# Performance work log

Measured on AMD Instinct MI355X. Metric: run time of the kernel, lower is better.

Reference implementation:

```python
import jax, jax.numpy as jnp
import numpy as np

P, N, NF = 4, 871, 512            # num_meta_paths, node_size (hardcoded 871 in source), node_feature_size
XDIM = 116 * 116                   # x_proj input dim, hardcoded Linear(116*116, nf)
BETA, LAMBDA_WL, GAMMA = 0.1, 0.1, 0.1


def _xavier(k, shape):
    fan_in, fan_out = shape[0], shape[-1]
    bound = np.sqrt(6.0 / (fan_in + fan_out))
    return jax.random.uniform(k, shape, jnp.float32, -bound, bound)


def setup_inputs() -> dict:
    key = jax.random.key(0)
    ks = jax.random.split(key, 12)
    return {
        "z_stack": jax.random.normal(ks[0], (P, N, NF), jnp.float32),
        "x_orig": jax.random.normal(ks[1], (1, 116, 116), jnp.float32),
        "W": _xavier(ks[2], (N, 1)),
        "b": jax.random.uniform(ks[3], (N, 1), jnp.float32),
        "q": _xavier(ks[4], (N, NF)),
        "xp_w": _xavier(ks[5], (XDIM, NF)),
        "xp_b": jnp.zeros((NF,), jnp.float32),
        "w1": _xavier(ks[6], (2 * NF, 512)), "b1": jnp.zeros((512,), jnp.float32),
        "w2": _xavier(ks[7], (512, 256)), "b2": jnp.zeros((256,), jnp.float32),
        "w3": _xavier(ks[8], (256, 1)), "b3": jnp.zeros((1,), jnp.float32),
        "perm": jax.random.permutation(ks[9], N).astype(jnp.int32),
    }


def _mi_mlp(t, w1, b1, w2, b2, w3, b3):
    h = jax.nn.relu(t @ w1 + b1)
    h = jax.nn.relu(h @ w2 + b2)
    return h @ w3 + b3  # [N, 1]


def reference(z_stack, x_orig, W, b, q, xp_w, xp_b, w1, b1, w2, b2, w3, b3, perm):
    # --- vectorized form of the per-node loop:
    # score_p = mean_i( tanh(W_i * z[p,i,:] + b_i) . q_i )
    zt = jnp.tanh(W[None] * z_stack + b[None])            # [P,N,NF]
    scores = jnp.mean(jnp.sum(zt * q[None], axis=-1), axis=-1)  # [P]
    proportions = scores / jnp.sum(scores)
    attn = jax.nn.softmax(proportions)                    # [P] (no isomorphic pairs -> no overwrite)
    # layer_out_p = attn_p * z_p + z_p ; emb = sum_p layer_out_p
    emb = jnp.einsum('p,pnf->nf', 1.0 + attn, z_stack)    # [N,NF]
    # --- estimate_MI(x_orig, emb, mi_estimator_xz)
    x = jnp.broadcast_to(x_orig.reshape(1, -1), (N, XDIM))
    xh = x @ xp_w + xp_b                                  # [N,NF]
    t0 = jnp.concatenate([xh, emb], axis=1)               # [N,2NF]
    t1 = jnp.concatenate([xh, emb[perm]], axis=1)
    mi_lb = jnp.mean(_mi_mlp(t0, w1, b1, w2, b2, w3, b3)) - jnp.log(
        jnp.mean(jnp.exp(_mi_mlp(t1, w1, b1, w2, b2, w3, b3))) + 1e-8)
    I_XZ = jnp.clip(mi_lb, 0.0)
    # y_labels=None -> I_ZY = 0 ; empty isomorphic_pairs -> wl_loss = 0
    total_loss = I_XZ - BETA * 0.0 + LAMBDA_WL * 0.0 + GAMMA * jnp.sum(attn)
    return emb, total_loss
```

## Files before the change

kernel.cpp:

```cpp
#include <hip/hip_runtime.h>
#include <hip/hip_bf16.h>
#include <math.h>

#define NMETA  4
#define NNODE  871
#define NFEAT  512
#define XDIM   (116*116)
#define ZPLANE (NNODE*NFEAT)
#define MT     55

#define NXB    254
#define XROWS  53

#define WS_CNT    12
#define WS_SPART  16
#define WS_C1P    256
#define WS_XHP    2560
#define WS_V      132608
#define WS_W1P    133504
#define WS_W2P    264576
#define WS_FXHP   297344
#define MAGICF    0x13579BDFu

typedef short v8s __attribute__((ext_vector_type(8)));
typedef float v4f __attribute__((ext_vector_type(4)));

static __device__ __forceinline__ short f2bf(float f) {
  __hip_bfloat16 h = __float2bfloat16(f);
  return *reinterpret_cast<short*>(&h);
}

static __device__ __forceinline__ unsigned ldflag(const float* ws, int off) {
  return __hip_atomic_load((const unsigned*)&ws[off], __ATOMIC_RELAXED,
                           __HIP_MEMORY_SCOPE_AGENT);
}
static __device__ __forceinline__ void stflag(float* ws, int off) {
  __builtin_amdgcn_fence(__ATOMIC_RELEASE, "agent");
  __hip_atomic_store((unsigned*)&ws[off], MAGICF, __ATOMIC_RELAXED,
                     __HIP_MEMORY_SCOPE_AGENT);
}

__global__ __launch_bounds__(1024) void k_front(const float* __restrict__ x,
                                                const float* __restrict__ xpw,
                                                const float* __restrict__ w1,
                                                const float* __restrict__ w2,
                                                const float* __restrict__ z,
                                                const float* __restrict__ W,
                                                const float* __restrict__ b,
                                                const float* __restrict__ q,
                                                const float* __restrict__ xpb,
                                                const float* __restrict__ b1,
                                                float* __restrict__ ws,
                                                short* __restrict__ w1p,
                                                short* __restrict__ w2p) {
  const int blk = blockIdx.x;
  const int tid = threadIdx.x;

  if (blk < NXB) {
    const int d0 = blk * XROWS;
    const int rows = min(XROWS, XDIM - d0);
    __shared__ float xs[XROWS];
    __shared__ float4 redx[7][128];
    if (tid < rows) xs[tid] = x[d0 + tid];
    __syncthreads();
    const int f4 = tid & 127;
    const int g = tid >> 7;
    float4 acc = {0.f, 0.f, 0.f, 0.f};
    const float4* xp4 = (const float4*)xpw;
    for (int r = g; r < rows; r += 8) {
      const float xv = xs[r];
      const float4 wv = xp4[(size_t)(d0 + r) * 128 + f4];
      acc.x += xv * wv.x; acc.y += xv * wv.y; acc.z += xv * wv.z; acc.w += xv * wv.w;
    }
    if (g) redx[g - 1][f4] = acc;
    __syncthreads();
    if (!g) {
#pragma unroll
      for (int k = 0; k < 7; ++k) {
        float4 t = redx[k][f4];
        acc.x += t.x; acc.y += t.y; acc.z += t.z; acc.w += t.w;
      }
      ((float4*)(ws + WS_XHP + (size_t)blk * 512))[f4] = acc;
    }
    __syncthreads();
    if (tid == 0) stflag(ws, WS_FXHP + blk);
  } else if (blk < NXB + MT) {
    const int sb = blk - NXB;
    const int row = tid >> 6;
    const int oc = tid & 63;
    const int gr = sb * 16 + row;
    const bool valid = gr < NNODE;
    const float4* z4 = (const float4*)z;
    const float4* q4 = (const float4*)q;
    float4 za0, za1, zb0, zb1, zc0, zc1, zd0, zd1, qa, qb;
    float wi = 0.f, bi = 0.f;
    za0 = za1 = zb0 = zb1 = zc0 = zc1 = zd0 = zd1 = (float4){0,0,0,0};
    qa = qb = (float4){0,0,0,0};
    const int zi = gr * 128 + oc * 2;
    if (valid) {
      za0 = z4[zi];                 za1 = z4[zi + 1];
      zb0 = z4[NNODE*128 + zi];     zb1 = z4[NNODE*128 + zi + 1];
      zc0 = z4[2*NNODE*128 + zi];   zc1 = z4[2*NNODE*128 + zi + 1];
      zd0 = z4[3*NNODE*128 + zi];   zd1 = z4[3*NNODE*128 + zi + 1];
      qa  = q4[zi];                 qb  = q4[zi + 1];
      wi = W[gr]; bi = b[gr];
    }
    auto dot8 = [&](const float4& u0, const float4& u1) -> float {
      return tanhf(wi*u0.x + bi)*qa.x + tanhf(wi*u0.y + bi)*qa.y
           + tanhf(wi*u0.z + bi)*qa.z + tanhf(wi*u0.w + bi)*qa.w
           + tanhf(wi*u1.x + bi)*qb.x + tanhf(wi*u1.y + bi)*qb.y
           + tanhf(wi*u1.z + bi)*qb.z + tanhf(wi*u1.w + bi)*qb.w;
    };
    float sp0 = valid ? dot8(za0, za1) : 0.f;
    float sp1 = valid ? dot8(zb0, zb1) : 0.f;
    float sp2 = valid ? dot8(zc0, zc1) : 0.f;
    float sp3 = valid ? dot8(zd0, zd1) : 0.f;
#pragma unroll
    for (int m = 1; m < 64; m <<= 1) {
      sp0 += __shfl_xor(sp0, m); sp1 += __shfl_xor(sp1, m);
      sp2 += __shfl_xor(sp2, m); sp3 += __shfl_xor(sp3, m);
    }
    __shared__ float sred[16][4];
    if (oc == 0) {
      sred[row][0] = sp0; sred[row][1] = sp1;
      sred[row][2] = sp2; sred[row][3] = sp3;
    }
    __syncthreads();
    if (tid < 4) {
      float s = 0.f;
#pragma unroll
      for (int r = 0; r < 16; ++r) s += sred[r][tid];
      ws[WS_SPART + tid * 55 + sb] = s;
    }
  } else if (blk < NXB + MT + 20) {
    const int pb = blk - (NXB + MT);
    if (pb < 16) {
      const int s0 = pb * 16384;
#pragma unroll
      for (int it = 0; it < 16; ++it) {
        const int s = s0 + it * 1024 + tid;
        const int k = s >> 9, n = s & 511;
        const int t = (k >> 5) * 16384 + (n >> 4) * 512 + ((k >> 3) & 3) * 128
                    + (n & 15) * 8 + (k & 7);
        w1p[t] = f2bf(w1[(size_t)(512 + k) * 512 + n]);
      }
    } else {
      const int o0 = (pb - 16) * 16384;
#pragma unroll
      for (int it = 0; it < 16; ++it) {
        const int o = o0 + it * 1024 + tid;
        const int k = o >> 8, n = o & 255;
        const int t = (k >> 5) * 8192 + (n >> 4) * 512 + ((k >> 3) & 3) * 128
                    + (n & 15) * 8 + (k & 7);
        w2p[t] = f2bf(w2[(size_t)k * 256 + n]);
      }
    }
  } else {
    const int bk = blk - (NXB + MT + 20);
    __shared__ float xh[128];
    __shared__ float redr[1024];
    __shared__ float4 redg[7][128];
    if (tid == 1023) *(unsigned*)&ws[WS_CNT] = 0u;
    for (;;) {
      int ok = 1;
      if (tid < NXB) ok = (ldflag(ws, WS_FXHP + tid) == MAGICF);
      if (__syncthreads_and(ok)) break;
      __builtin_amdgcn_s_sleep(2);
    }
    __builtin_amdgcn_fence(__ATOMIC_ACQUIRE, "agent");
    const int f = tid & 127;
    const int part = tid >> 7;
    {
      float s = 0.f;
      for (int p = part; p < NXB; p += 8)
        s += ws[WS_XHP + (size_t)p * 512 + bk * 128 + f];
      redr[tid] = s;
    }
    __syncthreads();
    if (tid < 128) {
      float t = xpb[bk * 128 + tid];
#pragma unroll
      for (int g = 0; g < 8; ++g) t += redr[g * 128 + tid];
      xh[tid] = t;
    }
    __syncthreads();
    const int j4 = tid & 127;
    const int fg = tid >> 7;
    float4 acc = {0.f, 0.f, 0.f, 0.f};
    const float4* w14 = (const float4*)w1;
#pragma unroll
    for (int ff = 0; ff < 16; ++ff) {
      const int fr = bk * 128 + fg * 16 + ff;
      const float xv = xh[fg * 16 + ff];
      const float4 wv = w14[(size_t)fr * 128 + j4];
      acc.x += xv * wv.x; acc.y += xv * wv.y; acc.z += xv * wv.z; acc.w += xv * wv.w;
    }
    if (fg) redg[fg - 1][j4] = acc;
    __syncthreads();
    if (!fg) {
#pragma unroll
      for (int g = 0; g < 7; ++g) {
        float4 t = redg[g][j4];
        acc.x += t.x; acc.y += t.y; acc.z += t.z; acc.w += t.w;
      }
      if (bk == 0) {
        acc.x += b1[j4 * 4 + 0]; acc.y += b1[j4 * 4 + 1];
        acc.z += b1[j4 * 4 + 2]; acc.w += b1[j4 * 4 + 3];
      }
      ((float4*)(ws + WS_C1P + (size_t)bk * 512))[j4] = acc;
    }
  }
}

__global__ __launch_bounds__(1024) void k_fused(const float* __restrict__ z,
                                                float* __restrict__ ws,
                                                float* __restrict__ out,
                                                const short* __restrict__ w1p,
                                                const short* __restrict__ w2p,
                                                const float* __restrict__ b2,
                                                const float* __restrict__ w3,
                                                const float* __restrict__ b3) {
  __shared__ __align__(16) short embs[8192];
  __shared__ __align__(16) short h2a[8192];
  __shared__ float cs[512];
  __shared__ float rf0[1024], rf1[1024];
  __shared__ float vred[16][17];
  __shared__ float cf[4];
  __shared__ float svred[4];
  const int tid = threadIdx.x;
  const int r0 = blockIdx.x * 16;
  const int oc = tid & 63;
  const int row = tid >> 6;
  const int gr = r0 + row;
  const bool valid = gr < NNODE;

  const float4* z4 = (const float4*)z;
  float4 za0, za1, zb0, zb1, zc0, zc1, zd0, zd1;
  za0 = za1 = zb0 = zb1 = zc0 = zc1 = zd0 = zd1 = (float4){0,0,0,0};
  const int zi = gr * 128 + oc * 2;
  if (valid) {
    za0 = z4[zi];                 za1 = z4[zi + 1];
    zb0 = z4[NNODE*128 + zi];     zb1 = z4[NNODE*128 + zi + 1];
    zc0 = z4[2*NNODE*128 + zi];   zc1 = z4[2*NNODE*128 + zi + 1];
    zd0 = z4[3*NNODE*128 + zi];   zd1 = z4[3*NNODE*128 + zi + 1];
  }

  if (tid < 512) {
    float a = 0.f;
#pragma unroll
    for (int k = 0; k < 4; ++k) a += ws[WS_C1P + k * 512 + tid];
    cs[tid] = a;
  }

  {
    const int w4 = tid >> 6;
    if (w4 < 4) {
      float v = (oc < 55) ? ws[WS_SPART + w4 * 55 + oc] : 0.f;
#pragma unroll
      for (int m = 1; m < 64; m <<= 1) v += __shfl_xor(v, m);
      if (oc == 0) svred[w4] = v;
    }
  }
  __syncthreads();
  if (tid == 0) {
    float sv[NMETA], sum = 0.f;
#pragma unroll
    for (int p = 0; p < NMETA; ++p) { sv[p] = svred[p] / (float)NNODE; sum += sv[p]; }
    float m = -1e30f;
#pragma unroll
    for (int p = 0; p < NMETA; ++p) { sv[p] = sv[p] / sum; m = fmaxf(m, sv[p]); }
    float es = 0.f;
#pragma unroll
    for (int p = 0; p < NMETA; ++p) { sv[p] = expf(sv[p] - m); es += sv[p]; }
#pragma unroll
    for (int p = 0; p < NMETA; ++p) cf[p] = 1.f + sv[p] / es;
  }
  __syncthreads();
  const float c0 = cf[0], c1c = cf[1], c2 = cf[2], c3 = cf[3];

  {
    const int slot = oc * 16 + (row ^ (oc & 15));
    v8s h;
    if (valid) {
      float4 r0v, r1v;
      r0v.x = c0*za0.x + c1c*zb0.x + c2*zc0.x + c3*zd0.x;
      r0v.y = c0*za0.y + c1c*zb0.y + c2*zc0.y + c3*zd0.y;
      r0v.z = c0*za0.z + c1c*zb0.z + c2*zc0.z + c3*zd0.z;
      r0v.w = c0*za0.w + c1c*zb0.w + c2*zc0.w + c3*zd0.w;
      r1v.x = c0*za1.x + c1c*zb1.x + c2*zc1.x + c3*zd1.x;
      r1v.y = c0*za1.y + c1c*zb1.y + c2*zc1.y + c3*zd1.y;
      r1v.z = c0*za1.z + c1c*zb1.z + c2*zc1.z + c3*zd1.z;
      r1v.w = c0*za1.w + c1c*zb1.w + c2*zc1.w + c3*zd1.w;
      ((float4*)out)[zi] = r0v;
      ((float4*)out)[zi + 1] = r1v;
      h[0] = f2bf(r0v.x); h[1] = f2bf(r0v.y); h[2] = f2bf(r0v.z); h[3] = f2bf(r0v.w);
      h[4] = f2bf(r1v.x); h[5] = f2bf(r1v.y); h[6] = f2bf(r1v.z); h[7] = f2bf(r1v.w);
    } else {
      h = (v8s){0,0,0,0,0,0,0,0};
    }
    *(v8s*)(embs + slot * 8) = h;
  }
  __syncthreads();

  const int lane = tid & 63, w = tid >> 6;
  const int n15 = lane & 15, quad = lane >> 4;
  v4f e[2];
#pragma unroll
  for (int ct = 0; ct < 2; ++ct) e[ct] = (v4f){0.f, 0.f, 0.f, 0.f};
#pragma unroll
  for (int kb = 0; kb < 16; ++kb) {
    const int koct = kb * 4 + quad;
    v8s a = *(const v8s*)(embs + (koct * 16 + (n15 ^ (koct & 15))) * 8);
    const short* B = w1p + kb * 16384 + w * 1024 + quad * 128 + n15 * 8;
#pragma unroll
    for (int ct = 0; ct < 2; ++ct) {
      v8s bb = *(const v8s*)(B + ct * 512);
      e[ct] = __builtin_amdgcn_mfma_f32_16x16x32_bf16(a, bb, e[ct], 0, 0, 0);
    }
  }
#pragma unroll
  for (int ct = 0; ct < 2; ++ct) {
    const int col = w * 32 + ct * 16 + n15;
    const int koct = col >> 3, j = col & 7;
#pragma unroll
    for (int r = 0; r < 4; ++r) {
      const int m = quad * 4 + r;
      h2a[(koct * 16 + (m ^ (koct & 15))) * 8 + j] = f2bf(fmaxf(e[ct][r] + cs[col], 0.f));
    }
  }
  __syncthreads();

  v4f g = (v4f){0.f, 0.f, 0.f, 0.f};
#pragma unroll
  for (int kb = 0; kb < 16; ++kb) {
    const int koct = kb * 4 + quad;
    v8s a = *(const v8s*)(h2a + (koct * 16 + (n15 ^ (koct & 15))) * 8);
    v8s bb = *(const v8s*)(w2p + kb * 8192 + w * 512 + quad * 128 + n15 * 8);
    g = __builtin_amdgcn_mfma_f32_16x16x32_bf16(a, bb, g, 0, 0, 0);
  }
  {
    const int col = w * 16 + n15;
    const float b2v = b2[col], w3v = w3[col];
#pragma unroll
    for (int r = 0; r < 4; ++r) {
      float s = fmaxf(g[r] + b2v, 0.f) * w3v;
      s += __shfl_xor(s, 1);
      s += __shfl_xor(s, 2);
      s += __shfl_xor(s, 4);
      s += __shfl_xor(s, 8);
      if (n15 == 0) vred[quad * 4 + r][w] = s;
    }
  }
  __syncthreads();
  if (tid < 16) {
    float acc = 0.f;
#pragma unroll
    for (int ww = 0; ww < 16; ++ww) acc += vred[tid][ww];
    const int grow = r0 + tid;
    if (grow < NNODE) ws[WS_V + grow] = acc;
  }

  __shared__ unsigned last;
  __syncthreads();
  if (tid == 0) {
    __threadfence();
    unsigned old = atomicAdd((unsigned int*)&ws[WS_CNT], 1u);
    last = (old == MT - 1) ? 1u : 0u;
  }
  __syncthreads();
  if (last) {
    __builtin_amdgcn_fence(__ATOMIC_ACQUIRE, "agent");
    const float bias = b3[0];
    float s0 = 0.f, s1 = 0.f;
    for (int i = tid; i < NNODE; i += 1024) {
      float xv = ws[WS_V + i] + bias;
      s0 += xv;
      s1 += expf(xv);
    }
    rf0[tid] = s0; rf1[tid] = s1;
    __syncthreads();
    for (int s = 512; s > 0; s >>= 1) {
      if (tid < s) { rf0[tid] += rf0[tid + s]; rf1[tid] += rf1[tid + s]; }
      __syncthreads();
    }
    if (tid == 0) {
      float m0 = rf0[0] / (float)NNODE;
      float m1 = rf1[0] / (float)NNODE;
      float mi = m0 - logf(m1 + 1e-8f);
      out[ZPLANE] = fmaxf(mi, 0.f) + 0.1f;
    }
  }
}

extern "C" void kernel_launch(void* const* d_in, const int* in_sizes, int n_in,
                              void* d_out, int out_size, void* d_ws, size_t ws_size,
                              hipStream_t stream) {
  const float* z   = (const float*)d_in[0];
  const float* x   = (const float*)d_in[1];
  const float* W   = (const float*)d_in[2];
  const float* b   = (const float*)d_in[3];
  const float* q   = (const float*)d_in[4];
  const float* xpw = (const float*)d_in[5];
  const float* xpb = (const float*)d_in[6];
  const float* w1  = (const float*)d_in[7];
  const float* b1  = (const float*)d_in[8];
  const float* w2  = (const float*)d_in[9];
  const float* b2  = (const float*)d_in[10];
  const float* w3  = (const float*)d_in[11];
  const float* b3  = (const float*)d_in[12];
  float* out = (float*)d_out;
  float* ws  = (float*)d_ws;

  short* w1p = (short*)(ws + WS_W1P);
  short* w2p = (short*)(ws + WS_W2P);

  k_front<<<NXB + MT + 20 + 4, 1024, 0, stream>>>(x, xpw, w1, w2, z, W, b, q,
                                                  xpb, b1, ws, w1p, w2p);
  k_fused<<<MT, 1024, 0, stream>>>(z, ws, out, w1p, w2p, b2, w3, b3);
}
```

Baseline: 143.8 us.

## Replace in-kernel flag spin-wait with separate k_mid kernel launch

```diff
diff --git a/kernel.cpp b/kernel.cpp
--- a/kernel.cpp
+++ b/kernel.cpp
@@ -19,8 +19,6 @@
 #define WS_V      132608
 #define WS_W1P    133504
 #define WS_W2P    264576
-#define WS_FXHP   297344
-#define MAGICF    0x13579BDFu
 
 typedef short v8s __attribute__((ext_vector_type(8)));
 typedef float v4f __attribute__((ext_vector_type(4)));
@@ -28,16 +26,6 @@
 static __device__ __forceinline__ short f2bf(float f) {
   __hip_bfloat16 h = __float2bfloat16(f);
   return *reinterpret_cast<short*>(&h);
-}
-
-static __device__ __forceinline__ unsigned ldflag(const float* ws, int off) {
-  return __hip_atomic_load((const unsigned*)&ws[off], __ATOMIC_RELAXED,
-                           __HIP_MEMORY_SCOPE_AGENT);
-}
-static __device__ __forceinline__ void stflag(float* ws, int off) {
-  __builtin_amdgcn_fence(__ATOMIC_RELEASE, "agent");
-  __hip_atomic_store((unsigned*)&ws[off], MAGICF, __ATOMIC_RELAXED,
-                     __HIP_MEMORY_SCOPE_AGENT);
 }
 
 __global__ __launch_bounds__(1024) void k_front(const float* __restrict__ x,
@@ -48,8 +36,6 @@
                                                 const float* __restrict__ W,
                                                 const float* __restrict__ b,
                                                 const float* __restrict__ q,
-                                                const float* __restrict__ xpb,
-                                                const float* __restrict__ b1,
                                                 float* __restrict__ ws,
                                                 short* __restrict__ w1p,
                                                 short* __restrict__ w2p) {
@@ -82,8 +68,6 @@
       }
       ((float4*)(ws + WS_XHP + (size_t)blk * 512))[f4] = acc;
     }
-    __syncthreads();
-    if (tid == 0) stflag(ws, WS_FXHP + blk);
   } else if (blk < NXB + MT) {
     const int sb = blk - NXB;
     const int row = tid >> 6;
@@ -132,7 +116,7 @@
       for (int r = 0; r < 16; ++r) s += sred[r][tid];
       ws[WS_SPART + tid * 55 + sb] = s;
     }
-  } else if (blk < NXB + MT + 20) {
+  } else {
     const int pb = blk - (NXB + MT);
     if (pb < 16) {
       const int s0 = pb * 16384;
@@ -155,60 +139,62 @@
         w2p[t] = f2bf(w2[(size_t)k * 256 + n]);
       }
     }
-  } else {
-    const int bk = blk - (NXB + MT + 20);
-    __shared__ float xh[128];
-    __shared__ float redr[1024];
-    __shared__ float4 redg[7][128];
-    if (tid == 1023) *(unsigned*)&ws[WS_CNT] = 0u;
-    for (;;) {
-      int ok = 1;
-      if (tid < NXB) ok = (ldflag(ws, WS_FXHP + tid) == MAGICF);
-      if (__syncthreads_and(ok)) break;
-      __builtin_amdgcn_s_sleep(2);
-    }
-    __builtin_amdgcn_fence(__ATOMIC_ACQUIRE, "agent");
-    const int f = tid & 127;
-    const int part = tid >> 7;
-    {
-      float s = 0.f;
-      for (int p = part; p < NXB; p += 8)
-        s += ws[WS_XHP + (size_t)p * 512 + bk * 128 + f];
-      redr[tid] = s;
-    }
-    __syncthreads();
-    if (tid < 128) {
-      float t = xpb[bk * 128 + tid];
-#pragma unroll
-      for (int g = 0; g < 8; ++g) t += redr[g * 128 + tid];
-      xh[tid] = t;
-    }
-    __syncthreads();
-    const int j4 = tid & 127;
-    const int fg = tid >> 7;
-    float4 acc = {0.f, 0.f, 0.f, 0.f};
-    const float4* w14 = (const float4*)w1;
-#pragma unroll
-    for (int ff = 0; ff < 16; ++ff) {
-      const int fr = bk * 128 + fg * 16 + ff;
-      const float xv = xh[fg * 16 + ff];
-      const float4 wv = w14[(size_t)fr * 128 + j4];
-      acc.x += xv * wv.x; acc.y += xv * wv.y; acc.z += xv * wv.z; acc.w += xv * wv.w;
-    }
-    if (fg) redg[fg - 1][j4] = acc;
-    __syncthreads();
-    if (!fg) {
-#pragma unroll
-      for (int g = 0; g < 7; ++g) {
-        float4 t = redg[g][j4];
-        acc.x += t.x; acc.y += t.y; acc.z += t.z; acc.w += t.w;
-      }
-      if (bk == 0) {
-        acc.x += b1[j4 * 4 + 0]; acc.y += b1[j4 * 4 + 1];
-        acc.z += b1[j4 * 4 + 2]; acc.w += b1[j4 * 4 + 3];
-      }
-      ((float4*)(ws + WS_C1P + (size_t)bk * 512))[j4] = acc;
-    }
+  }
+}
+
+__global__ __launch_bounds__(1024) void k_mid(const float* __restrict__ xpb,
+                                              const float* __restrict__ w1,
+                                              const float* __restrict__ b1,
+                                              float* __restrict__ ws) {
+  const int tid = threadIdx.x;
+  if (blockIdx.x == 4) {
+    if (tid == 0) *(unsigned*)&ws[WS_CNT] = 0u;
+    return;
+  }
+  const int bk = blockIdx.x;
+  __shared__ float xh[128];
+  __shared__ float redr[1024];
+  __shared__ float4 redg[7][128];
+  const int f = tid & 127;
+  const int part = tid >> 7;
+  {
+    float s = 0.f;
+    for (int p = part; p < NXB; p += 8)
+      s += ws[WS_XHP + (size_t)p * 512 + bk * 128 + f];
+    redr[tid] = s;
+  }
+  __syncthreads();
+  if (tid < 128) {
+    float t = xpb[bk * 128 + tid];
+#pragma unroll
+    for (int g = 0; g < 8; ++g) t += redr[g * 128 + tid];
+    xh[tid] = t;
+  }
+  __syncthreads();
+  const int j4 = tid & 127;
+  const int fg = tid >> 7;
+  float4 acc = {0.f, 0.f, 0.f, 0.f};
+  const float4* w14 = (const float4*)w1;
+#pragma unroll
+  for (int ff = 0; ff < 16; ++ff) {
+    const int fr = bk * 128 + fg * 16 + ff;
+    const float xv = xh[fg * 16 + ff];
+    const float4 wv = w14[(size_t)fr * 128 + j4];
+    acc.x += xv * wv.x; acc.y += xv * wv.y; acc.z += xv * wv.z; acc.w += xv * wv.w;
+  }
+  if (fg) redg[fg - 1][j4] = acc;
+  __syncthreads();
+  if (!fg) {
+#pragma unroll
+    for (int g = 0; g < 7; ++g) {
+      float4 t = redg[g][j4];
+      acc.x += t.x; acc.y += t.y; acc.z += t.z; acc.w += t.w;
+    }
+    if (bk == 0) {
+      acc.x += b1[j4 * 4 + 0]; acc.y += b1[j4 * 4 + 1];
+      acc.z += b1[j4 * 4 + 2]; acc.w += b1[j4 * 4 + 3];
+    }
+    ((float4*)(ws + WS_C1P + (size_t)bk * 512))[j4] = acc;
   }
 }
 
@@ -414,7 +400,8 @@
   short* w1p = (short*)(ws + WS_W1P);
   short* w2p = (short*)(ws + WS_W2P);
 
-  k_front<<<NXB + MT + 20 + 4, 1024, 0, stream>>>(x, xpw, w1, w2, z, W, b, q,
-                                                  xpb, b1, ws, w1p, w2p);
+  k_front<<<NXB + MT + 20, 1024, 0, stream>>>(x, xpw, w1, w2, z, W, b, q,
+                                              ws, w1p, w2p);
+  k_mid<<<5, 1024, 0, stream>>>(xpb, w1, b1, ws);
   k_fused<<<MT, 1024, 0, stream>>>(z, ws, out, w1p, w2p, b2, w3, b3);
 }
```

After: 139.9 us. 2.7% less time.
